# Performance work log

Hardware: AMD Instinct MI355X
Metric: run time of the kernel (lower is better)

The kernel has to match this reference:

```python
import jax, jax.numpy as jnp
import numpy as np

VOCAB = 256
EMBED = 1024
HIDDEN = 1024
LAYERS = 2
RATIO = 0.25
R_GATE = int(4 * HIDDEN * RATIO)   # low-rank dim of the 4H gate projection
R_DEC = int(VOCAB * RATIO)         # low-rank dim of decoder
BATCH, SEQ = 64, 256


def setup_inputs() -> dict:
    key = jax.random.key(0)
    ks = jax.random.split(key, 16)
    stdv = 1.0 / np.sqrt(HIDDEN)
    u = lambda k, shape, s: jax.random.uniform(k, shape, jnp.float32, -s, s)
    tokens = jax.random.randint(ks[0], (BATCH, SEQ), 0, VOCAB)
    embed = jax.random.normal(ks[1], (VOCAB, EMBED), jnp.float32)
    # per-layer low-rank LSTM params, stacked over layers (embed==hidden)
    VT_ih = u(ks[2], (LAYERS, R_GATE, HIDDEN), stdv)
    bVT_ih = u(ks[3], (LAYERS, R_GATE), stdv)
    U_ih = u(ks[4], (LAYERS, 4 * HIDDEN, R_GATE), stdv)
    bU_ih = u(ks[5], (LAYERS, 4 * HIDDEN), stdv)
    VT_hh = u(ks[6], (LAYERS, R_GATE, HIDDEN), stdv)
    bVT_hh = u(ks[7], (LAYERS, R_GATE), stdv)
    U_hh = u(ks[8], (LAYERS, 4 * HIDDEN, R_GATE), stdv)
    bU_hh = u(ks[9], (LAYERS, 4 * HIDDEN), stdv)
    # decoder LowRankLinear (nn.Linear default-ish init scale)
    s1 = 1.0 / np.sqrt(HIDDEN)
    s2 = 1.0 / np.sqrt(R_DEC)
    dec_VT = u(ks[10], (R_DEC, HIDDEN), s1)
    dec_bVT = u(ks[11], (R_DEC,), s1)
    dec_U = u(ks[12], (VOCAB, R_DEC), s2)
    dec_bU = u(ks[13], (VOCAB,), s2)
    return dict(tokens=tokens, embed=embed, VT_ih=VT_ih, bVT_ih=bVT_ih,
                U_ih=U_ih, bU_ih=bU_ih, VT_hh=VT_hh, bVT_hh=bVT_hh,
                U_hh=U_hh, bU_hh=bU_hh, dec_VT=dec_VT, dec_bVT=dec_bVT,
                dec_U=dec_U, dec_bU=dec_bU)


def _lstm_layer(x_seq, p):
    # x_seq: [T, B, H]; p: tuple of this layer's params
    vt_ih, bvt_ih, u_ih, bu_ih, vt_hh, bvt_hh, u_hh, bu_hh = p
    B = x_seq.shape[1]
    H = u_ih.shape[0] // 4
    h0 = jnp.zeros((B, H), x_seq.dtype)
    c0 = jnp.zeros((B, H), x_seq.dtype)

    def step(carry, x):
        h, c = carry
        gates = ((x @ vt_ih.T + bvt_ih) @ u_ih.T + bu_ih
                 + (h @ vt_hh.T + bvt_hh) @ u_hh.T + bu_hh)   # [B, 4H]
        i, f, g, o = jnp.split(gates, 4, axis=-1)
        i = jax.nn.sigmoid(i)
        f = jax.nn.sigmoid(f)
        g = jnp.tanh(g)
        o = jax.nn.sigmoid(o)
        c_new = f * c + i * g
        h_new = o * jnp.tanh(c_new)
        return (h_new, c_new), h_new

    _, out = jax.lax.scan(step, (h0, c0), x_seq)
    return out  # [T, B, H]


def reference(tokens, embed, VT_ih, bVT_ih, U_ih, bU_ih, VT_hh, bVT_hh,
              U_hh, bU_hh, dec_VT, dec_bVT, dec_U, dec_bU):
    x = embed[tokens]                 # [B, T, E]
    x = jnp.transpose(x, (1, 0, 2))   # time-major [T, B, E]
    for l in range(LAYERS):
        p = (VT_ih[l], bVT_ih[l], U_ih[l], bU_ih[l],
             VT_hh[l], bVT_hh[l], U_hh[l], bU_hh[l])
        x = _lstm_layer(x, p)
    # low-rank decoder: [T, B, H] -> [T, B, V]
    logits = (x @ dec_VT.T + dec_bVT) @ dec_U.T + dec_bU
    return jnp.transpose(logits, (1, 2, 0))  # [B, V, T]
```

## Files before the change

### kernel.cpp

```cpp
#include <hip/hip_runtime.h>
#include <hip/hip_bf16.h>


#define B_SZ   64
#define T_SEQ  256
#define HID    1024
#define G4     4096

typedef __attribute__((ext_vector_type(8))) short bf16x8;
typedef __attribute__((ext_vector_type(4))) float f32x4;
typedef __attribute__((ext_vector_type(4))) short bf16x4;
typedef unsigned long long u64;

__device__ __forceinline__ f32x4 mfma16(bf16x8 a, bf16x8 b, f32x4 c) {
  return __builtin_amdgcn_mfma_f32_16x16x32_bf16(a, b, c, 0, 0, 0);
}
__device__ __forceinline__ float sigm(float x)  { return 1.f / (1.f + __expf(-x)); }
__device__ __forceinline__ float tanh_(float x) { return 2.f / (1.f + __expf(-2.f * x)) - 1.f; }
__device__ __forceinline__ f32x4 fzero() { f32x4 z; z[0]=0.f; z[1]=0.f; z[2]=0.f; z[3]=0.f; return z; }

__device__ __forceinline__ bf16x8 lda(const __hip_bfloat16* p) {
  const u64* q = (const u64*)p;
  union { u64 u[2]; bf16x8 v; } r;
  r.u[0] = __hip_atomic_load(q,     __ATOMIC_RELAXED, __HIP_MEMORY_SCOPE_AGENT);
  r.u[1] = __hip_atomic_load(q + 1, __ATOMIC_RELAXED, __HIP_MEMORY_SCOPE_AGENT);
  return r.v;
}

__device__ __forceinline__ float ld1(const void* p, size_t i, int mode) {
  return mode ? ((const float*)p)[i]
              : __bfloat162float(((const __hip_bfloat16*)p)[i]);
}
__device__ __forceinline__ bf16x8 ld8(const void* p, size_t i, int mode) {
  if (mode) {
    const float* f = (const float*)p + i;
    float4 a = *(const float4*)f;
    float4 b = *(const float4*)(f + 4);
    union { bf16x8 v; __hip_bfloat16 h[8]; } u;
    u.h[0] = __float2bfloat16(a.x); u.h[1] = __float2bfloat16(a.y);
    u.h[2] = __float2bfloat16(a.z); u.h[3] = __float2bfloat16(a.w);
    u.h[4] = __float2bfloat16(b.x); u.h[5] = __float2bfloat16(b.y);
    u.h[6] = __float2bfloat16(b.z); u.h[7] = __float2bfloat16(b.w);
    return u.v;
  }
  return *(const bf16x8*)((const __hip_bfloat16*)p + i);
}

__global__ void k_detect(const unsigned short* __restrict__ e, int* __restrict__ flags) {
  __shared__ int cnt;
  if (threadIdx.x == 0) cnt = 0;
  __syncthreads();
  int c = 0;
  for (int i = threadIdx.x; i < 2048; i += 256) {
    unsigned int bits = ((unsigned int)e[2 * i]) << 16;
    float f = __uint_as_float(bits);
    if (!isfinite(f) || fabsf(f) > 1e10f) ++c;
  }
  atomicAdd(&cnt, c);
  __syncthreads();
  if (threadIdx.x == 0) flags[0] = (cnt > 8) ? 1 : 0;
}

__global__ void k_cvt_b(const void* __restrict__ src, __hip_bfloat16* __restrict__ dst,
                        int n, const int* __restrict__ flags) {
  const int mode = flags[0];
  for (int i = blockIdx.x * blockDim.x + threadIdx.x; i < n; i += gridDim.x * blockDim.x)
    dst[i] = mode ? __float2bfloat16(((const float*)src)[i])
                  : ((const __hip_bfloat16*)src)[i];
}
__global__ void k_cvt_f(const void* __restrict__ src, float* __restrict__ dst,
                        int n, const int* __restrict__ flags) {
  const int mode = flags[0];
  for (int i = blockIdx.x * blockDim.x + threadIdx.x; i < n; i += gridDim.x * blockDim.x)
    dst[i] = mode ? ((const float*)src)[i]
                  : __bfloat162float(((const __hip_bfloat16*)src)[i]);
}

__global__ void k_init(unsigned* bar) {
  for (int i = threadIdx.x; i < 1024; i += 256) bar[i] = 0u;
}

__global__ void __launch_bounds__(256) k_combine(
    const void* __restrict__ U_ih, const void* __restrict__ U_hh,
    const void* __restrict__ VT_ih, const void* __restrict__ VT_hh,
    __hip_bfloat16* __restrict__ Wc, const int* __restrict__ flags)
{
  __shared__ __hip_bfloat16 sB[4 * 64 * 8];
  const int mode = flags[0];
  const int idx  = blockIdx.x;
  const int Mid  = idx >> 10;
  const int rem  = idx & 1023;
  const int gblk = rem >> 4, kblk = rem & 15;
  const int L = Mid >> 1, typ = Mid & 1;
  const void* U  = typ ? U_hh  : U_ih;
  const void* VT = typ ? VT_hh : VT_ih;
  const size_t Uoff  = (size_t)L * G4 * HID;
  const size_t VToff = (size_t)L * HID * HID;
  const int tid = threadIdx.x, lane = tid & 63, wv = tid >> 6;

  f32x4 acc[4];
  for (int i = 0; i < 4; ++i) acc[i] = fzero();

  const int r_local = tid >> 3;
  const int kk8     = (tid & 7) * 8;

  for (int r0 = 0; r0 < HID; r0 += 32) {
    union { bf16x8 v; __hip_bfloat16 h[8]; } u;
    u.v = ld8(VT, VToff + (size_t)(r0 + r_local) * HID + kblk * 64 + kk8, mode);
    __syncthreads();
    #pragma unroll
    for (int j = 0; j < 8; ++j) {
      int k_local = kk8 + j;
      int tile = k_local >> 4;
      int ln   = ((r_local >> 3) << 4) | (k_local & 15);
      sB[(tile * 64 + ln) * 8 + (r_local & 7)] = u.h[j];
    }
    __syncthreads();
    bf16x8 a = ld8(U, Uoff + (size_t)(gblk * 64 + wv * 16 + (lane & 15)) * HID
                          + r0 + (lane >> 4) * 8, mode);
    #pragma unroll
    for (int nt = 0; nt < 4; ++nt) {
      bf16x8 b = *(const bf16x8*)(sB + (nt * 64 + lane) * 8);
      acc[nt] = mfma16(a, b, acc[nt]);
    }
  }
  #pragma unroll
  for (int nt = 0; nt < 4; ++nt)
    #pragma unroll
    for (int r = 0; r < 4; ++r) {
      int g = gblk * 64 + wv * 16 + (lane >> 4) * 4 + r;
      int k = kblk * 64 + nt * 16 + (lane & 15);
      Wc[((size_t)Mid * G4 + g) * HID + k] = __float2bfloat16(acc[nt][r]);
    }
}

__global__ void __launch_bounds__(256) k_bias(
    const void* __restrict__ bVT_ih, const void* __restrict__ U_ih,
    const void* __restrict__ bU_ih,
    const void* __restrict__ bVT_hh, const void* __restrict__ U_hh,
    const void* __restrict__ bU_hh,
    float* __restrict__ bc, const int* __restrict__ flags)
{
  const int mode  = flags[0];
  const int g_all = blockIdx.x * 4 + (threadIdx.x >> 6);
  const int lane  = threadIdx.x & 63;
  const int L = g_all >> 12, g = g_all & 4095;
  const size_t ub = (size_t)(L * G4 + g) * HID + lane * 16;
  const size_t vb = (size_t)L * HID + lane * 16;
  float s = 0.f;
  #pragma unroll
  for (int c = 0; c < 16; ++c)
    s += ld1(bVT_ih, vb + c, mode) * ld1(U_ih, ub + c, mode)
       + ld1(bVT_hh, vb + c, mode) * ld1(U_hh, ub + c, mode);
  for (int off = 32; off; off >>= 1) s += __shfl_down(s, off);
  if (lane == 0)
    bc[g_all] = s + ld1(bU_ih, L * G4 + g, mode) + ld1(bU_hh, L * G4 + g, mode);
}

__global__ void __launch_bounds__(256, 1) k_lstm(
    const int* __restrict__ tokens, const __hip_bfloat16* __restrict__ embedC,
    const __hip_bfloat16* __restrict__ Wc, const float* __restrict__ bc,
    __hip_bfloat16* __restrict__ H1, __hip_bfloat16* __restrict__ H2,
    unsigned* bar, const int h1mask, const int cmode)
{
  extern __shared__ char smem[];
  __hip_bfloat16* Wl = (__hip_bfloat16*)smem;
  f32x4* Xex = (f32x4*)(smem + 131072);
  __hip_bfloat16* Hs = (__hip_bfloat16*)(smem + 147456);

  const int tid  = threadIdx.x;
  const int lane = tid & 63, wv = tid >> 6;
  const int w    = blockIdx.x;
  const int L    = w >> 7, jg = w & 127;
  const int mat  = wv >> 1, mhalf = wv & 1;
  const bool leaderWave = (jg == 0) && (wv == 0);

  for (int q = tid; q < 8192; q += 256) {
    int m_ = q >> 12, ks = (q >> 7) & 31, tl = (q >> 6) & 1, ln = q & 63;
    int n_local = tl * 16 + (ln & 15);
    int g = (n_local >> 3) * 1024 + jg * 8 + (n_local & 7);
    int k = ks * 32 + (ln >> 4) * 8;
    *(bf16x8*)(Wl + (size_t)q * 8) =
        *(const bf16x8*)(Wc + (((size_t)(L * 2 + m_) * G4 + g) << 10) + k);
  }
  const int nb = lane & 7;
  const float b_i = bc[L * G4 +        jg * 8 + nb];
  const float b_f = bc[L * G4 + 1024 + jg * 8 + nb];
  const float b_g = bc[L * G4 + 2048 + jg * 8 + nb];
  const float b_o = bc[L * G4 + 3072 + jg * 8 + nb];
  __syncthreads();

  float cst[2][4] = {{0.f,0.f,0.f,0.f},{0.f,0.f,0.f,0.f}};
  const int m0 = mhalf * 32 + (lane & 15);
  const int ko = (lane >> 4) * 8;
  const __hip_bfloat16* wbase = Wl + mat * 32768;
  unsigned* Xrel = bar + 256 + L * 128;

  for (int t = 0; t < T_SEQ; ++t) {
    f32x4* XexB = Xex + ((t & 1) << 9);
    __hip_bfloat16* HsB = Hs + ((t & 1) << 9);

    if (leaderWave) {
      const u64* own = (const u64*)bar + (L ? 64 : 0);
      const u64* oth = (const u64*)bar + (L ? 0 : 64);
      const unsigned need = (unsigned)t;
      for (;;) {
        u64 a = __hip_atomic_load(&own[lane], __ATOMIC_RELAXED, __HIP_MEMORY_SCOPE_AGENT);
        bool ok = ((unsigned)a >= need) && ((unsigned)(a >> 32) >= need);
        if (L == 1) {
          u64 b = __hip_atomic_load(&oth[lane], __ATOMIC_RELAXED, __HIP_MEMORY_SCOPE_AGENT);
          ok = ok && ((unsigned)b >= need + 1) && ((unsigned)(b >> 32) >= need + 1);
        } else if (cmode == 0) {
          u64 b = __hip_atomic_load(&oth[lane], __ATOMIC_RELAXED, __HIP_MEMORY_SCOPE_AGENT);
          ok = ok && ((unsigned)b + 3u >= need) && ((unsigned)(b >> 32) + 3u >= need);
        }
        if (__all(ok)) break;
        __builtin_amdgcn_s_sleep(1);
      }
      if (lane < 8)
        __hip_atomic_store(&Xrel[lane * 16], (unsigned)(t + 1),
                           __ATOMIC_RELAXED, __HIP_MEMORY_SCOPE_AGENT);
    } else if (L == 1 || mat == 1) {
      if (lane == 0) {
        for (;;) {
          unsigned v = __hip_atomic_load(&Xrel[(w & 7) * 16],
                                         __ATOMIC_RELAXED, __HIP_MEMORY_SCOPE_AGENT);
          if (v >= (unsigned)(t + 1)) break;
          __builtin_amdgcn_s_sleep(2);
        }
      }
    }

    f32x4 acc00 = fzero(), acc01 = fzero(), acc10 = fzero(), acc11 = fzero();
    bool doGemm = true, cached = false;
    const __hip_bfloat16 *A0 = nullptr, *A1 = nullptr;
    if (mat == 0) {
      if (L == 0) {
        A0 = embedC + ((size_t)tokens[m0 * T_SEQ + t] << 10);
        A1 = embedC + ((size_t)tokens[(m0 + 16) * T_SEQ + t] << 10);
        cached = true;
      } else {
        A0 = H1 + ((((size_t)(t & h1mask)) * 64 + m0) << 10);
        A1 = A0 + ((size_t)16 << 10);
        cached = (cmode != 0);
      }
    } else {
      if (t == 0) doGemm = false;
      else {
        if (L == 0) {
          A0 = H1 + ((((size_t)((t - 1) & h1mask)) * 64 + m0) << 10);
          cached = (cmode != 0);
        } else {
          A0 = H2 + (((size_t)(t - 1) * 64 + m0) << 10);
          cached = true;
        }
        A1 = A0 + ((size_t)16 << 10);
      }
    }
    if (doGemm) {
      if (cached) {
        bf16x8 p0[32], p1[32];
        #pragma unroll
        for (int i = 0; i < 32; ++i) {
          p0[i] = *(const bf16x8*)(A0 + i * 32 + ko);
          p1[i] = *(const bf16x8*)(A1 + i * 32 + ko);
        }
        __builtin_amdgcn_sched_barrier(0);
        #pragma unroll
        for (int ks = 0; ks < 32; ++ks) {
          bf16x8 b0 = *(const bf16x8*)(wbase + (ks * 2 + 0) * 512 + lane * 8);
          bf16x8 b1 = *(const bf16x8*)(wbase + (ks * 2 + 1) * 512 + lane * 8);
          acc00 = mfma16(p0[ks], b0, acc00);
          acc01 = mfma16(p0[ks], b1, acc01);
          acc10 = mfma16(p1[ks], b0, acc10);
          acc11 = mfma16(p1[ks], b1, acc11);
        }
      } else {
        #pragma unroll 4
        for (int ks = 0; ks < 32; ++ks) {
          bf16x8 a0 = lda(A0 + ks * 32 + ko);
          bf16x8 a1 = lda(A1 + ks * 32 + ko);
          bf16x8 b0 = *(const bf16x8*)(wbase + (ks * 2 + 0) * 512 + lane * 8);
          bf16x8 b1 = *(const bf16x8*)(wbase + (ks * 2 + 1) * 512 + lane * 8);
          acc00 = mfma16(a0, b0, acc00);
          acc01 = mfma16(a0, b1, acc01);
          acc10 = mfma16(a1, b0, acc10);
          acc11 = mfma16(a1, b1, acc11);
        }
      }
    }
    if (mat == 0) {
      XexB[(mhalf * 4 + 0) * 64 + lane] = acc00;
      XexB[(mhalf * 4 + 1) * 64 + lane] = acc01;
      XexB[(mhalf * 4 + 2) * 64 + lane] = acc10;
      XexB[(mhalf * 4 + 3) * 64 + lane] = acc11;
    }
    __syncthreads();
    if (mat == 1) {
      #pragma unroll
      for (int mt = 0; mt < 2; ++mt) {
        f32x4 aT0 = mt ? acc10 : acc00;
        f32x4 aT1 = mt ? acc11 : acc01;
        f32x4 gx0 = XexB[(mhalf * 4 + mt * 2 + 0) * 64 + lane];
        f32x4 gx1 = XexB[(mhalf * 4 + mt * 2 + 1) * 64 + lane];
        #pragma unroll
        for (int r = 0; r < 4; ++r) {
          float v0 = aT0[r] + gx0[r];
          float v1 = aT1[r] + gx1[r];
          float p0 = __shfl_xor(v0, 8);
          float p1 = __shfl_xor(v1, 8);
          if ((lane & 15) < 8) {
            float iv = sigm(v0 + b_i);
            float fv = sigm(p0 + b_f);
            float gv = tanh_(v1 + b_g);
            float ov = sigm(p1 + b_o);
            float c  = fv * cst[mt][r] + iv * gv;
            cst[mt][r] = c;
            float h  = ov * tanh_(c);
            int m = mhalf * 32 + mt * 16 + (lane >> 4) * 4 + r;
            HsB[m * 8 + (lane & 15)] = __float2bfloat16(h);
          }
        }
      }
    }
    __syncthreads();
    if (wv == 0) {
      char* HoutB = (L == 0) ? (char*)(H1 + (((size_t)(t & h1mask)) << 16))
                             : (char*)(H2 + (((size_t)t) << 16));
      const u64* HsQ = (const u64*)HsB;
      #pragma unroll
      for (int q = 0; q < 2; ++q) {
        int i = lane + q * 64;
        u64 v = HsQ[i];
        u64* dst = (u64*)(HoutB + ((size_t)(i >> 1) << 11) + (jg << 4) + ((i & 1) << 3));
        __hip_atomic_store(dst, v, __ATOMIC_RELAXED, __HIP_MEMORY_SCOPE_AGENT);
      }
      asm volatile("s_waitcnt vmcnt(0)" ::: "memory");
      if (lane == 0)
        __hip_atomic_store(&bar[w], (unsigned)(t + 1),
                           __ATOMIC_RELAXED, __HIP_MEMORY_SCOPE_AGENT);
    }
  }
}

__global__ void __launch_bounds__(256) k_dec1(
    const __hip_bfloat16* __restrict__ H2, const __hip_bfloat16* __restrict__ dec_VTC,
    const float* __restrict__ dbv, __hip_bfloat16* __restrict__ R)
{
  const int t = blockIdx.x;
  const int lane = threadIdx.x & 63, wv = threadIdx.x >> 6;
  const __hip_bfloat16* A = H2 + ((size_t)t << 16) + ((size_t)(wv * 16 + (lane & 15)) << 10);
  const int ko = (lane >> 4) * 8;
  f32x4 acc[4];
  for (int i = 0; i < 4; ++i) acc[i] = fzero();
  for (int ks = 0; ks < 32; ++ks) {
    bf16x8 a = *(const bf16x8*)(A + ks * 32 + ko);
    #pragma unroll
    for (int nt = 0; nt < 4; ++nt) {
      bf16x8 b = *(const bf16x8*)(dec_VTC + ((size_t)(nt * 16 + (lane & 15)) << 10) + ks * 32 + ko);
      acc[nt] = mfma16(a, b, acc[nt]);
    }
  }
  #pragma unroll
  for (int nt = 0; nt < 4; ++nt) {
    int n = nt * 16 + (lane & 15);
    float bias = dbv[n];
    #pragma unroll
    for (int r = 0; r < 4; ++r) {
      int b_row = wv * 16 + (lane >> 4) * 4 + r;
      R[((size_t)t << 12) + (size_t)b_row * 64 + n] = __float2bfloat16(acc[nt][r] + bias);
    }
  }
}

__global__ void __launch_bounds__(256) k_dec2(
    const __hip_bfloat16* __restrict__ R, const __hip_bfloat16* __restrict__ dec_UC,
    const float* __restrict__ dbu, void* __restrict__ out,
    const int* __restrict__ flags)
{
  const int mode = flags[0];
  const int bblk = blockIdx.x >> 4, tblk = blockIdx.x & 15;
  const int lane = threadIdx.x & 63, wv = threadIdx.x >> 6;
  const int ko  = (lane >> 4) * 8;
  const int t_l = lane & 15;
  for (int bi = 0; bi < 4; ++bi) {
    const int b = bblk * 16 + wv * 4 + bi;
    f32x4 acc[16];
    for (int i = 0; i < 16; ++i) acc[i] = fzero();
    #pragma unroll
    for (int ks = 0; ks < 2; ++ks) {
      bf16x8 a = *(const bf16x8*)(R + (((size_t)(tblk * 16 + t_l) * 64 + b) << 6)
                                    + ks * 32 + ko);
      #pragma unroll
      for (int nt = 0; nt < 16; ++nt) {
        bf16x8 bb = *(const bf16x8*)(dec_UC + ((size_t)(nt * 16 + t_l) << 6) + ks * 32 + ko);
        acc[nt] = mfma16(a, bb, acc[nt]);
      }
    }
    #pragma unroll
    for (int nt = 0; nt < 16; ++nt) {
      int v = nt * 16 + t_l;
      float bias = dbu[v];
      size_t off = (size_t)b * 65536 + (size_t)v * 256 + tblk * 16 + (lane >> 4) * 4;
      if (mode) {
        float4 st;
        st.x = acc[nt][0] + bias; st.y = acc[nt][1] + bias;
        st.z = acc[nt][2] + bias; st.w = acc[nt][3] + bias;
        *(float4*)((float*)out + off) = st;
      } else {
        union { bf16x4 v4; __hip_bfloat16 h[4]; } u;
        #pragma unroll
        for (int r = 0; r < 4; ++r) u.h[r] = __float2bfloat16(acc[nt][r] + bias);
        *(bf16x4*)((__hip_bfloat16*)out + off) = u.v4;
      }
    }
  }
}

extern "C" void kernel_launch(void* const* d_in, const int* in_sizes, int n_in,
                              void* d_out, int out_size, void* d_ws, size_t ws_size,
                              hipStream_t stream)
{
  const int* tokens  = (const int*)d_in[0];
  const void* embed  = d_in[1];
  const void* VT_ih  = d_in[2];
  const void* bVT_ih = d_in[3];
  const void* U_ih   = d_in[4];
  const void* bU_ih  = d_in[5];
  const void* VT_hh  = d_in[6];
  const void* bVT_hh = d_in[7];
  const void* U_hh   = d_in[8];
  const void* bU_hh  = d_in[9];
  const void* dec_VT = d_in[10];
  const void* dec_bVT= d_in[11];
  const void* dec_U  = d_in[12];
  const void* dec_bU = d_in[13];

  char* ws = (char*)d_ws;
  const size_t M = 1024 * 1024;
  __hip_bfloat16* Wc      = (__hip_bfloat16*)ws;
  __hip_bfloat16* H2      = (__hip_bfloat16*)(ws + 32 * M);
  char* aux = ws + 64 * M;
  int*            flags   = (int*)aux;
  float*          bc      = (float*)(aux + 4096);
  float*          dbv     = (float*)(aux + 36864);
  float*          dbu     = (float*)(aux + 37120);
  __hip_bfloat16* embedC  = (__hip_bfloat16*)(aux + 65536);
  __hip_bfloat16* dec_VTC = (__hip_bfloat16*)(aux + 589824);
  __hip_bfloat16* dec_UC  = (__hip_bfloat16*)(aux + 720896);
  __hip_bfloat16* H1ring  = (__hip_bfloat16*)(aux + 1048576);
  unsigned*       bar     = (unsigned*)(aux + 1572864);
  __hip_bfloat16* R       = (__hip_bfloat16*)(aux + 2097152);
  __hip_bfloat16* H1big   = (__hip_bfloat16*)(ws + 68 * M);

  (void)in_sizes; (void)n_in; (void)out_size;

  const int big = (ws_size >= (size_t)100 * M);
  __hip_bfloat16* H1 = big ? H1big : H1ring;
  const int h1mask = big ? 255 : 3;
  const int cmode  = big ? 1 : 0;

  hipFuncSetAttribute((const void*)k_lstm,
                      hipFuncAttributeMaxDynamicSharedMemorySize, 149504);

  k_detect<<<1, 256, 0, stream>>>((const unsigned short*)embed, flags);
  k_cvt_b<<<256, 256, 0, stream>>>(embed,  embedC,  256 * 1024, flags);
  k_cvt_b<<<64,  256, 0, stream>>>(dec_VT, dec_VTC, 64 * 1024,  flags);
  k_cvt_b<<<16,  256, 0, stream>>>(dec_U,  dec_UC,  256 * 64,   flags);
  k_cvt_f<<<1,   64,  0, stream>>>(dec_bVT, dbv, 64,  flags);
  k_cvt_f<<<1,   256, 0, stream>>>(dec_bU,  dbu, 256, flags);
  k_combine<<<4096, 256, 0, stream>>>(U_ih, U_hh, VT_ih, VT_hh, Wc, flags);
  k_bias   <<<2048, 256, 0, stream>>>(bVT_ih, U_ih, bU_ih, bVT_hh, U_hh, bU_hh, bc, flags);
  k_init   <<<1, 256, 0, stream>>>(bar);
  k_lstm   <<<256, 256, 149504, stream>>>(tokens, embedC, Wc, bc, H1, H2, bar,
                                          h1mask, cmode);
  k_dec1   <<<256, 256, 0, stream>>>(H2, dec_VTC, dbv, R);
  k_dec2   <<<64, 256, 0, stream>>>(R, dec_UC, dbu, d_out, flags);
}
```

Measured before the change: 3.396 ms.

## Remove block-wide sync before h publish and stagger K order across blocks

The final __syncthreads is removed. Each mat==1 wave now writes its own half of the new hidden rows to global memory and sets a separate per-half flag, so the barrier array is doubled and the waiting leader checks both flag sets. The Xrel release flags are spread over 32 slots instead of 8 to reduce contention. The K loop start is rotated by block index (jg) so blocks read different slices of the shared h/x rows at the same moment, which spreads cache and channel pressure. The risk is more polling traffic on the doubled flag set and a possible ordering hazard on the shared Hs buffer now that the sync is gone.

```diff
diff --git a/kernel.cpp b/kernel.cpp
--- a/kernel.cpp
+++ b/kernel.cpp
@@ -77,7 +77,7 @@
 }
 
 __global__ void k_init(unsigned* bar) {
-  for (int i = threadIdx.x; i < 1024; i += 256) bar[i] = 0u;
+  for (int i = threadIdx.x; i < 2048; i += 256) bar[i] = 0u;
 }
 
 __global__ void __launch_bounds__(256) k_combine(
@@ -194,36 +194,44 @@
   const int m0 = mhalf * 32 + (lane & 15);
   const int ko = (lane >> 4) * 8;
   const __hip_bfloat16* wbase = Wl + mat * 32768;
-  unsigned* Xrel = bar + 256 + L * 128;
+  unsigned* Xrel = bar + 1024 + L * 512;
 
   for (int t = 0; t < T_SEQ; ++t) {
     f32x4* XexB = Xex + ((t & 1) << 9);
     __hip_bfloat16* HsB = Hs + ((t & 1) << 9);
 
     if (leaderWave) {
-      const u64* own = (const u64*)bar + (L ? 64 : 0);
-      const u64* oth = (const u64*)bar + (L ? 0 : 64);
+      const u64* ownA = (const u64*)bar + (L ? 64 : 0);
+      const u64* ownB = (const u64*)bar + 128 + (L ? 64 : 0);
+      const u64* othA = (const u64*)bar + (L ? 0 : 64);
+      const u64* othB = (const u64*)bar + 128 + (L ? 0 : 64);
       const unsigned need = (unsigned)t;
       for (;;) {
-        u64 a = __hip_atomic_load(&own[lane], __ATOMIC_RELAXED, __HIP_MEMORY_SCOPE_AGENT);
-        bool ok = ((unsigned)a >= need) && ((unsigned)(a >> 32) >= need);
+        u64 a = __hip_atomic_load(&ownA[lane], __ATOMIC_RELAXED, __HIP_MEMORY_SCOPE_AGENT);
+        u64 b = __hip_atomic_load(&ownB[lane], __ATOMIC_RELAXED, __HIP_MEMORY_SCOPE_AGENT);
+        bool ok = ((unsigned)a >= need) && ((unsigned)(a >> 32) >= need)
+               && ((unsigned)b >= need) && ((unsigned)(b >> 32) >= need);
         if (L == 1) {
-          u64 b = __hip_atomic_load(&oth[lane], __ATOMIC_RELAXED, __HIP_MEMORY_SCOPE_AGENT);
-          ok = ok && ((unsigned)b >= need + 1) && ((unsigned)(b >> 32) >= need + 1);
+          u64 c = __hip_atomic_load(&othA[lane], __ATOMIC_RELAXED, __HIP_MEMORY_SCOPE_AGENT);
+          u64 d = __hip_atomic_load(&othB[lane], __ATOMIC_RELAXED, __HIP_MEMORY_SCOPE_AGENT);
+          ok = ok && ((unsigned)c >= need + 1) && ((unsigned)(c >> 32) >= need + 1)
+                  && ((unsigned)d >= need + 1) && ((unsigned)(d >> 32) >= need + 1);
         } else if (cmode == 0) {
-          u64 b = __hip_atomic_load(&oth[lane], __ATOMIC_RELAXED, __HIP_MEMORY_SCOPE_AGENT);
-          ok = ok && ((unsigned)b + 3u >= need) && ((unsigned)(b >> 32) + 3u >= need);
+          u64 c = __hip_atomic_load(&othA[lane], __ATOMIC_RELAXED, __HIP_MEMORY_SCOPE_AGENT);
+          u64 d = __hip_atomic_load(&othB[lane], __ATOMIC_RELAXED, __HIP_MEMORY_SCOPE_AGENT);
+          ok = ok && ((unsigned)c + 3u >= need) && ((unsigned)(c >> 32) + 3u >= need)
+                  && ((unsigned)d + 3u >= need) && ((unsigned)(d >> 32) + 3u >= need);
         }
         if (__all(ok)) break;
         __builtin_amdgcn_s_sleep(1);
       }
-      if (lane < 8)
+      if (lane < 32)
         __hip_atomic_store(&Xrel[lane * 16], (unsigned)(t + 1),
                            __ATOMIC_RELAXED, __HIP_MEMORY_SCOPE_AGENT);
     } else if (L == 1 || mat == 1) {
       if (lane == 0) {
         for (;;) {
-          unsigned v = __hip_atomic_load(&Xrel[(w & 7) * 16],
+          unsigned v = __hip_atomic_load(&Xrel[(w & 31) * 16],
                                          __ATOMIC_RELAXED, __HIP_MEMORY_SCOPE_AGENT);
           if (v >= (unsigned)(t + 1)) break;
           __builtin_amdgcn_s_sleep(2);
@@ -262,14 +270,16 @@
         bf16x8 p0[32], p1[32];
         #pragma unroll
         for (int i = 0; i < 32; ++i) {
-          p0[i] = *(const bf16x8*)(A0 + i * 32 + ko);
-          p1[i] = *(const bf16x8*)(A1 + i * 32 + ko);
+          int kp = (i + jg) & 31;
+          p0[i] = *(const bf16x8*)(A0 + kp * 32 + ko);
+          p1[i] = *(const bf16x8*)(A1 + kp * 32 + ko);
         }
         __builtin_amdgcn_sched_barrier(0);
         #pragma unroll
         for (int ks = 0; ks < 32; ++ks) {
-          bf16x8 b0 = *(const bf16x8*)(wbase + (ks * 2 + 0) * 512 + lane * 8);
-          bf16x8 b1 = *(const bf16x8*)(wbase + (ks * 2 + 1) * 512 + lane * 8);
+          int kp = (ks + jg) & 31;
+          bf16x8 b0 = *(const bf16x8*)(wbase + (kp * 2 + 0) * 512 + lane * 8);
+          bf16x8 b1 = *(const bf16x8*)(wbase + (kp * 2 + 1) * 512 + lane * 8);
           acc00 = mfma16(p0[ks], b0, acc00);
           acc01 = mfma16(p0[ks], b1, acc01);
           acc10 = mfma16(p1[ks], b0, acc10);
@@ -278,10 +288,11 @@
       } else {
         #pragma unroll 4
         for (int ks = 0; ks < 32; ++ks) {
-          bf16x8 a0 = lda(A0 + ks * 32 + ko);
-          bf16x8 a1 = lda(A1 + ks * 32 + ko);
-          bf16x8 b0 = *(const bf16x8*)(wbase + (ks * 2 + 0) * 512 + lane * 8);
-          bf16x8 b1 = *(const bf16x8*)(wbase + (ks * 2 + 1) * 512 + lane * 8);
+          int kp = (ks + jg) & 31;
+          bf16x8 a0 = lda(A0 + kp * 32 + ko);
+          bf16x8 a1 = lda(A1 + kp * 32 + ko);
+          bf16x8 b0 = *(const bf16x8*)(wbase + (kp * 2 + 0) * 512 + lane * 8);
+          bf16x8 b1 = *(const bf16x8*)(wbase + (kp * 2 + 1) * 512 + lane * 8);
           acc00 = mfma16(a0, b0, acc00);
           acc01 = mfma16(a0, b1, acc01);
           acc10 = mfma16(a1, b0, acc10);
@@ -322,23 +333,19 @@
           }
         }
       }
-    }
-    __syncthreads();
-    if (wv == 0) {
-      char* HoutB = (L == 0) ? (char*)(H1 + (((size_t)(t & h1mask)) << 16))
-                             : (char*)(H2 + (((size_t)t) << 16));
-      const u64* HsQ = (const u64*)HsB;
-      #pragma unroll
-      for (int q = 0; q < 2; ++q) {
-        int i = lane + q * 64;
-        u64 v = HsQ[i];
-        u64* dst = (u64*)(HoutB + ((size_t)(i >> 1) << 11) + (jg << 4) + ((i & 1) << 3));
+      {
+        char* HoutB = (L == 0) ? (char*)(H1 + (((size_t)(t & h1mask)) << 16))
+                               : (char*)(H2 + (((size_t)t) << 16));
+        const u64* HsQ = (const u64*)HsB;
+        u64 v = HsQ[mhalf * 64 + lane];
+        int row = mhalf * 32 + (lane >> 1);
+        u64* dst = (u64*)(HoutB + ((size_t)row << 11) + (jg << 4) + ((lane & 1) << 3));
         __hip_atomic_store(dst, v, __ATOMIC_RELAXED, __HIP_MEMORY_SCOPE_AGENT);
-      }
-      asm volatile("s_waitcnt vmcnt(0)" ::: "memory");
-      if (lane == 0)
-        __hip_atomic_store(&bar[w], (unsigned)(t + 1),
-                           __ATOMIC_RELAXED, __HIP_MEMORY_SCOPE_AGENT);
+        asm volatile("s_waitcnt vmcnt(0)" ::: "memory");
+        if (lane == 0)
+          __hip_atomic_store(&bar[mhalf * 256 + w], (unsigned)(t + 1),
+                             __ATOMIC_RELAXED, __HIP_MEMORY_SCOPE_AGENT);
+      }
     }
   }
 }
```

Result: slower. 3.581 ms (+5.5%).
